# Optimization experiments

Hardware: AMD Instinct MI355X
Metric: run time of the kernel (lower is better)

The kernel has to match this reference:

```python
import jax, jax.numpy as jnp
import numpy as np

B, S, D, H = 4, 2048, 1024, 16
DK = D // H
NEG = -1000000000.0


def setup_inputs() -> dict:
    key = jax.random.key(0)
    ks = jax.random.split(key, 12)
    scale = 1.0 / np.sqrt(D)
    inp = {
        "query": jax.random.normal(ks[0], (B, S, D), jnp.float32),
        "key": jax.random.normal(ks[1], (B, S, D), jnp.float32),
        "value": jax.random.normal(ks[2], (B, S, D), jnp.float32),
        "mask": jax.random.randint(ks[3], (B, S, S), 0, 2, jnp.int32),
        "Wq": jax.random.normal(ks[4], (D, D), jnp.float32) * scale,
        "bq": jnp.zeros((D,), jnp.float32),
        "Wk": jax.random.normal(ks[5], (D, D), jnp.float32) * scale,
        "bk": jnp.zeros((D,), jnp.float32),
        "Wv": jax.random.normal(ks[6], (D, D), jnp.float32) * scale,
        "bv": jnp.zeros((D,), jnp.float32),
        "Wo": jax.random.normal(ks[7], (D, D), jnp.float32) * scale,
        "bo": jnp.zeros((D,), jnp.float32),
    }
    return inp


def _split_heads(x):
    # (B, S, D) -> (B, H, S, DK)
    return x.reshape(B, -1, H, DK).transpose(0, 2, 1, 3)


def reference(query, key, value, mask, Wq, bq, Wk, bk, Wv, bv, Wo, bo):
    q = _split_heads(query @ Wq.T + bq)
    k = _split_heads(key @ Wk.T + bk)
    v = _split_heads(value @ Wv.T + bv)
    scores = jnp.einsum('bhqd,bhkd->bhqk', q, k) / jnp.sqrt(jnp.float32(DK))
    scores = jnp.where(mask[:, None, :, :] == 0, NEG, scores)
    p_attn = jax.nn.softmax(scores, axis=-1)
    x = jnp.einsum('bhqk,bhkd->bhqd', p_attn, v)
    x = x.transpose(0, 2, 1, 3).reshape(B, -1, D)
    return x @ Wo.T + bo
```

## Files before the change

### kernel.cpp

```cpp
#include <hip/hip_runtime.h>

#define BDIM 4
#define SDIM 2048
#define DDIM 1024
#define HDIM 16
#define DKDIM 64
#define MDIM (BDIM*SDIM)

typedef __attribute__((ext_vector_type(8))) short bf16x8_t;
typedef __attribute__((ext_vector_type(4))) float f32x4_t;

__device__ __forceinline__ unsigned short f2bf(float f) {
    union { float f; unsigned u; } v; v.f = f;
    unsigned r = v.u + 0x7FFFu + ((v.u >> 16) & 1u);
    return (unsigned short)(r >> 16);
}

__device__ __forceinline__ unsigned pkbf(float a, float b) {
#if defined(__has_builtin) && __has_builtin(__builtin_amdgcn_cvt_pk_bf16_f32)
    auto v = __builtin_amdgcn_cvt_pk_bf16_f32(a, b);
    union { decltype(v) x; unsigned u; } cv; cv.x = v; return cv.u;
#else
    return (unsigned)f2bf(a) | ((unsigned)f2bf(b) << 16);
#endif
}

#if defined(__has_builtin) && __has_builtin(__builtin_amdgcn_exp2f)
#define EXP2F(x) __builtin_amdgcn_exp2f(x)
#else
#define EXP2F(x) __expf((x) * 0.69314718f)
#endif

#define QSCALE 0.18033688011112042f

__device__ __forceinline__ void gl_lds16(const void* g, void* l) {
    __builtin_amdgcn_global_load_lds(
        (const __attribute__((address_space(1))) unsigned int*)g,
        (__attribute__((address_space(3))) unsigned int*)l, 16, 0, 0);
}

__global__ void cvt3(const float* __restrict__ a, const float* __restrict__ b, const float* __restrict__ c,
                     unsigned short* __restrict__ oa, unsigned short* __restrict__ ob, unsigned short* __restrict__ oc,
                     int n4) {
    int i = blockIdx.x * blockDim.x + threadIdx.x;
    const float* s = blockIdx.y == 0 ? a : (blockIdx.y == 1 ? b : c);
    unsigned short* d = blockIdx.y == 0 ? oa : (blockIdx.y == 1 ? ob : oc);
    if (i < n4) {
        float4 v = ((const float4*)s)[i];
        ushort4 o;
        o.x = f2bf(v.x); o.y = f2bf(v.y); o.z = f2bf(v.z); o.w = f2bf(v.w);
        ((ushort4*)d)[i] = o;
    }
}

__global__ void cvt4(const float* __restrict__ a, const float* __restrict__ b,
                     const float* __restrict__ c, const float* __restrict__ e,
                     unsigned short* __restrict__ oa, unsigned short* __restrict__ ob,
                     unsigned short* __restrict__ oc, unsigned short* __restrict__ oe,
                     int n4) {
    int i = blockIdx.x * blockDim.x + threadIdx.x;
    const float* s = blockIdx.y == 0 ? a : (blockIdx.y == 1 ? b : (blockIdx.y == 2 ? c : e));
    unsigned short* d = blockIdx.y == 0 ? oa : (blockIdx.y == 1 ? ob : (blockIdx.y == 2 ? oc : oe));
    if (i < n4) {
        float4 v = ((const float4*)s)[i];
        ushort4 o;
        o.x = f2bf(v.x); o.y = f2bf(v.y); o.z = f2bf(v.z); o.w = f2bf(v.w);
        ((ushort4*)d)[i] = o;
    }
}

__global__ void pack_mask(const int* __restrict__ m, unsigned long long* __restrict__ bits) {
    int g = blockIdx.x * 256 + threadIdx.x;
    unsigned long long bal = __ballot(m[g] != 0);
    if ((threadIdx.x & 63) == 0) bits[g >> 6] = bal;
}

template<int OMODE>
__global__ __launch_bounds__(256) void gemm_nt(
    const unsigned short* __restrict__ A,
    const unsigned short* __restrict__ B,
    const float* __restrict__ bias,
    unsigned short* __restrict__ Cb,
    float* __restrict__ Cf,
    int M, int N, int K, float scale)
{
    __shared__ unsigned short As[128 * 32];
    __shared__ unsigned short Bs[128 * 32];
    const int tid = threadIdx.x;
    const int w = tid >> 6, lane = tid & 63;
    const int wr = w >> 1, wc = w & 1;
    const int quad = lane >> 4, l16 = lane & 15;
    const int bn = blockIdx.x, bm = blockIdx.y;

    const int rl = lane >> 2;
    const int cl = (((lane & 3) ^ ((rl >> 1) & 3)) * 8);
    const int sw = (l16 >> 1) & 3;
    const int c0 = w * 2;
    const unsigned short* gA = A + (size_t)(bm * 128 + c0 * 16 + rl) * K + cl;
    const unsigned short* gB = B + (size_t)(bn * 128 + c0 * 16 + rl) * K + cl;
    unsigned short* lA = As + c0 * 512 + lane * 8;
    unsigned short* lB = Bs + c0 * 512 + lane * 8;

    f32x4_t acc[4][4] = {};

    for (int k0 = 0; k0 < K; k0 += 32) {
        gl_lds16(gA, lA);
        gl_lds16(gA + (size_t)16 * K, lA + 16 * 32);
        gl_lds16(gB, lB);
        gl_lds16(gB + (size_t)16 * K, lB + 16 * 32);
        gA += 32; gB += 32;
        __syncthreads();
        bf16x8_t af[4], bfr[4];
#pragma unroll
        for (int mi = 0; mi < 4; ++mi)
            af[mi] = *(const bf16x8_t*)(As + (wr * 64 + mi * 16 + l16) * 32 + (quad ^ sw) * 8);
#pragma unroll
        for (int ni = 0; ni < 4; ++ni)
            bfr[ni] = *(const bf16x8_t*)(Bs + (wc * 64 + ni * 16 + l16) * 32 + (quad ^ sw) * 8);
#pragma unroll
        for (int mi = 0; mi < 4; ++mi)
#pragma unroll
            for (int ni = 0; ni < 4; ++ni)
                acc[mi][ni] = __builtin_amdgcn_mfma_f32_16x16x32_bf16(af[mi], bfr[ni], acc[mi][ni], 0, 0, 0);
        __syncthreads();
    }

#pragma unroll
    for (int mi = 0; mi < 4; ++mi) {
#pragma unroll
        for (int ni = 0; ni < 4; ++ni) {
            const int n = bn * 128 + wc * 64 + ni * 16 + l16;
            const int m0 = bm * 128 + wr * 64 + mi * 16 + quad * 4;
            const float bv = bias[n];
            if (OMODE == 1) {
                ushort4 pk;
                pk.x = f2bf((acc[mi][ni][0] + bv) * scale);
                pk.y = f2bf((acc[mi][ni][1] + bv) * scale);
                pk.z = f2bf((acc[mi][ni][2] + bv) * scale);
                pk.w = f2bf((acc[mi][ni][3] + bv) * scale);
                *(ushort4*)(Cb + (size_t)n * M + m0) = pk;
            } else {
#pragma unroll
                for (int r = 0; r < 4; ++r) {
                    const float v = (acc[mi][ni][r] + bv) * scale;
                    if (OMODE == 0) Cb[(size_t)(m0 + r) * N + n] = f2bf(v);
                    else            Cf[(size_t)(m0 + r) * N + n] = v;
                }
            }
        }
    }
}

__global__ __launch_bounds__(256) void attn_kernel(
    const unsigned short* __restrict__ Qp,
    const unsigned short* __restrict__ Kp,
    const unsigned short* __restrict__ Vt,
    const unsigned long long* __restrict__ mbits,
    unsigned short* __restrict__ Xa)
{
    __shared__ unsigned short SMEM[8192];
    unsigned short* const Ks = SMEM;
    unsigned short* const Vs = SMEM + 4096;

    const int tid = threadIdx.x, w = tid >> 6, lane = tid & 63;
    const int quad = lane >> 4, l16 = lane & 15;
    const int bx = blockIdx.x;
    const int h = bx & 15, qt = (bx >> 4) & 15, b = bx >> 8;
    const int q0 = qt * 128;
    const int rl = lane >> 2;
    const int cl = (((lane & 3) ^ ((rl >> 1) & 3)) * 8);
    const int sw = (l16 >> 1) & 3;
    const bool hi16 = (lane & 16) != 0;
    const bool hi32 = (lane & 32) != 0;
    const int idxA = (2 * (quad & 1) + (quad >> 1)) * 16 + l16;
    const int idxC = idxA ^ 16;

#pragma unroll
    for (int i = 0; i < 4; ++i) {
        const int cc = w * 4 + i;
        const int row = b * SDIM + q0 + (cc & 7) * 16 + rl;
        const int col = h * 64 + (cc >> 3) * 32 + cl;
        gl_lds16(Qp + (size_t)row * DDIM + col, SMEM + cc * 512 + lane * 8);
    }
    __syncthreads();
    bf16x8_t aq[2][2];
#pragma unroll
    for (int g = 0; g < 2; ++g)
#pragma unroll
        for (int kk = 0; kk < 2; ++kk)
            aq[g][kk] = *(const bf16x8_t*)(SMEM + (kk * 8 + w * 2 + g) * 512 + l16 * 32 + (quad ^ sw) * 8);

    const unsigned long long* mq0 = mbits + (size_t)(b * SDIM + q0 + w * 32 + l16) * 32;
    const unsigned long long* mq1 = mq0 + (size_t)16 * 32;

    f32x4_t o[2][4] = {};
    f32x4_t o4[2] = {};
    union { unsigned u[4]; bf16x8_t v; } ones;
    ones.u[0] = ones.u[1] = ones.u[2] = ones.u[3] = 0x3F803F80u;

    for (int kt = 0; kt < SDIM / 64; ++kt) {
        __syncthreads();
#pragma unroll
        for (int i = 0; i < 2; ++i) {
            const int cc = w * 2 + i;
            const int rowk = b * SDIM + kt * 64 + (cc & 3) * 16 + rl;
            const int colk = h * 64 + (cc >> 2) * 32 + cl;
            gl_lds16(Kp + (size_t)rowk * DDIM + colk, Ks + cc * 512 + lane * 8);
            const int rowv = h * 64 + (cc & 3) * 16 + rl;
            const int colv = b * SDIM + kt * 64 + (cc >> 2) * 32 + cl;
            gl_lds16(Vt + (size_t)rowv * MDIM + colv, Vs + cc * 512 + lane * 8);
        }
        __syncthreads();

        const unsigned long long sh0 = mq0[kt] >> (quad * 4);
        const unsigned long long sh1 = mq1[kt] >> (quad * 4);

        f32x4_t sf[2][4] = {};
#pragma unroll
        for (int kk = 0; kk < 2; ++kk) {
#pragma unroll
            for (int ni = 0; ni < 4; ++ni) {
                const bf16x8_t ak = *(const bf16x8_t*)(Ks + kk * 2048 + (ni * 16 + l16) * 32 + (quad ^ sw) * 8);
                sf[0][ni] = __builtin_amdgcn_mfma_f32_16x16x32_bf16(ak, aq[0][kk], sf[0][ni], 0, 0, 0);
                sf[1][ni] = __builtin_amdgcn_mfma_f32_16x16x32_bf16(ak, aq[1][kk], sf[1][ni], 0, 0, 0);
            }
        }

        unsigned P[2][4][2];
#pragma unroll
        for (int g = 0; g < 2; ++g) {
            const unsigned long long s = g ? sh1 : sh0;
            const unsigned mlo = (unsigned)s, mhi = (unsigned)(s >> 32);
#pragma unroll
            for (int ni = 0; ni < 4; ++ni) {
                const unsigned msel = (ni < 2) ? mlo : mhi;
                const int shf = (ni & 1) * 16;
                float p[4];
#pragma unroll
                for (int r = 0; r < 4; ++r) {
                    const bool on = (msel >> (shf + r)) & 1u;
                    p[r] = EXP2F(on ? sf[g][ni][r] : -1.0e9f);
                }
                P[g][ni][0] = pkbf(p[0], p[1]);
                P[g][ni][1] = pkbf(p[2], p[3]);
            }
        }

#pragma unroll
        for (int kk2 = 0; kk2 < 2; ++kk2) {
            bf16x8_t va[4];
#pragma unroll
            for (int ni = 0; ni < 4; ++ni)
                va[ni] = *(const bf16x8_t*)(Vs + kk2 * 2048 + (ni * 16 + l16) * 32 + (quad ^ sw) * 8);
#pragma unroll
            for (int g = 0; g < 2; ++g) {
                const unsigned Pa = P[g][kk2 * 2][0], Pb = P[g][kk2 * 2][1];
                const unsigned Pc = P[g][kk2 * 2 + 1][0], Pd = P[g][kk2 * 2 + 1][1];
                const int RA = hi16 ? (int)Pc : (int)Pa;
                const int RB = hi16 ? (int)Pd : (int)Pb;
                const int RC = hi16 ? (int)Pa : (int)Pc;
                const int RD = hi16 ? (int)Pb : (int)Pd;
                const int Av = __shfl(RA, idxA, 64);
                const int Bv = __shfl(RB, idxA, 64);
                const int Cv = __shfl(RC, idxC, 64);
                const int Dv = __shfl(RD, idxC, 64);
                union { unsigned u[4]; bf16x8_t v; } pf;
                pf.u[0] = (unsigned)(hi32 ? Cv : Av);
                pf.u[1] = (unsigned)(hi32 ? Dv : Bv);
                pf.u[2] = (unsigned)(hi32 ? Av : Cv);
                pf.u[3] = (unsigned)(hi32 ? Bv : Dv);
#pragma unroll
                for (int ni = 0; ni < 4; ++ni)
                    o[g][ni] = __builtin_amdgcn_mfma_f32_16x16x32_bf16(va[ni], pf.v, o[g][ni], 0, 0, 0);
                o4[g] = __builtin_amdgcn_mfma_f32_16x16x32_bf16(ones.v, pf.v, o4[g], 0, 0, 0);
            }
        }
    }

    __syncthreads();
    unsigned short* T = SMEM + w * 1152;
#pragma unroll
    for (int g = 0; g < 2; ++g) {
        const float rcp = 1.0f / o4[g][0];
#pragma unroll
        for (int ni = 0; ni < 4; ++ni) {
            uint2 pk;
            pk.x = pkbf(o[g][ni][0] * rcp, o[g][ni][1] * rcp);
            pk.y = pkbf(o[g][ni][2] * rcp, o[g][ni][3] * rcp);
            *(uint2*)&T[l16 * 72 + ni * 16 + quad * 4] = pk;
        }
        const int qrow = q0 + w * 32 + g * 16 + (lane >> 2);
        const int dkc = (lane & 3) * 16;
        const bf16x8_t r0 = *(const bf16x8_t*)&T[(lane >> 2) * 72 + dkc];
        const bf16x8_t r1 = *(const bf16x8_t*)&T[(lane >> 2) * 72 + dkc + 8];
        unsigned short* dst = Xa + (size_t)(b * SDIM + qrow) * DDIM + h * 64 + dkc;
        *(bf16x8_t*)dst = r0;
        *(bf16x8_t*)(dst + 8) = r1;
    }
}

extern "C" void kernel_launch(void* const* d_in, const int* in_sizes, int n_in,
                              void* d_out, int out_size, void* d_ws, size_t ws_size,
                              hipStream_t stream)
{
    const float* query = (const float*)d_in[0];
    const float* key   = (const float*)d_in[1];
    const float* value = (const float*)d_in[2];
    const int*   mask  = (const int*)d_in[3];
    const float* Wq = (const float*)d_in[4];  const float* bq = (const float*)d_in[5];
    const float* Wk = (const float*)d_in[6];  const float* bk = (const float*)d_in[7];
    const float* Wv = (const float*)d_in[8];  const float* bv = (const float*)d_in[9];
    const float* Wo = (const float*)d_in[10]; const float* bo = (const float*)d_in[11];

    const size_t MD = (size_t)MDIM * DDIM;
    const size_t DD = (size_t)DDIM * DDIM;

    unsigned short* qb  = (unsigned short*)d_ws;
    unsigned short* kb  = qb + MD;
    unsigned short* vb  = kb + MD;
    unsigned short* wqb = vb + MD;
    unsigned short* wkb = wqb + DD;
    unsigned short* wvb = wkb + DD;
    unsigned short* wob = wvb + DD;
    unsigned short* Qp  = wob + DD;
    unsigned short* Kp  = Qp + MD;
    unsigned short* Vt  = Kp + MD;
    unsigned short* Xa  = Vt + MD;
    unsigned long long* mbits = (unsigned long long*)qb;

    {
        const int n4m = (int)(MD / 4), n4d = (int)(DD / 4);
        dim3 g3((n4m + 255) / 256, 3), g4((n4d + 255) / 256, 4);
        cvt3<<<g3, 256, 0, stream>>>(query, key, value, qb, kb, vb, n4m);
        cvt4<<<g4, 256, 0, stream>>>(Wq, Wk, Wv, Wo, wqb, wkb, wvb, wob, n4d);
    }

    dim3 gg(DDIM / 128, MDIM / 128);
    gemm_nt<0><<<gg, 256, 0, stream>>>(qb, wqb, bq, Qp, nullptr, MDIM, DDIM, DDIM, QSCALE);
    gemm_nt<0><<<gg, 256, 0, stream>>>(kb, wkb, bk, Kp, nullptr, MDIM, DDIM, DDIM, 1.0f);
    gemm_nt<1><<<gg, 256, 0, stream>>>(vb, wvb, bv, Vt, nullptr, MDIM, DDIM, DDIM, 1.0f);

    pack_mask<<<(BDIM * SDIM * SDIM) / 256, 256, 0, stream>>>(mask, mbits);

    attn_kernel<<<BDIM * HDIM * (SDIM / 128), 256, 0, stream>>>(Qp, Kp, Vt, mbits, Xa);

    gemm_nt<2><<<gg, 256, 0, stream>>>(Xa, wob, bo, nullptr, (float*)d_out, MDIM, DDIM, DDIM, 1.0f);
}
```

Before: 490.2 us.

## Double-buffer LDS in GEMMs and attention, batch QKV projections in one launch

Adds double-buffered shared memory to the GEMM and attention loops so the global-to-LDS load of the next K tile (and next K/V tile plus mask words) is issued before computing on the current one, removing one barrier per iteration. The three Q/K/V projection GEMMs are merged into a single launch using blockIdx.z to select operands. The output GEMM becomes its own specialized kernel. The cost is doubled LDS per block, which may lower occupancy, plus extra barriers in the attention epilogue.

Result: faster. 463.8 us (-5.4%).

```diff
diff --git a/kernel.cpp b/kernel.cpp
--- a/kernel.cpp
+++ b/kernel.cpp
@@ -75,17 +75,25 @@
     if ((threadIdx.x & 63) == 0) bits[g >> 6] = bal;
 }
 
-template<int OMODE>
-__global__ __launch_bounds__(256) void gemm_nt(
-    const unsigned short* __restrict__ A,
-    const unsigned short* __restrict__ B,
-    const float* __restrict__ bias,
-    unsigned short* __restrict__ Cb,
-    float* __restrict__ Cf,
-    int M, int N, int K, float scale)
+__global__ __launch_bounds__(256) void gemm_qkv(
+    const unsigned short* __restrict__ A0, const unsigned short* __restrict__ A1,
+    const unsigned short* __restrict__ A2,
+    const unsigned short* __restrict__ B0, const unsigned short* __restrict__ B1,
+    const unsigned short* __restrict__ B2,
+    const float* __restrict__ bi0, const float* __restrict__ bi1, const float* __restrict__ bi2,
+    unsigned short* __restrict__ C0, unsigned short* __restrict__ C1,
+    unsigned short* __restrict__ C2)
 {
-    __shared__ unsigned short As[128 * 32];
-    __shared__ unsigned short Bs[128 * 32];
+    __shared__ unsigned short As[2][128 * 32];
+    __shared__ unsigned short Bs[2][128 * 32];
+    const int K = DDIM, M = MDIM, N = DDIM;
+    const int z = blockIdx.z;
+    const unsigned short* A = z == 0 ? A0 : (z == 1 ? A1 : A2);
+    const unsigned short* Bw = z == 0 ? B0 : (z == 1 ? B1 : B2);
+    const float* bias = z == 0 ? bi0 : (z == 1 ? bi1 : bi2);
+    unsigned short* Cb = z == 0 ? C0 : (z == 1 ? C1 : C2);
+    const float scale = z == 0 ? QSCALE : 1.0f;
+
     const int tid = threadIdx.x;
     const int w = tid >> 6, lane = tid & 63;
     const int wr = w >> 1, wc = w & 1;
@@ -97,32 +105,40 @@
     const int sw = (l16 >> 1) & 3;
     const int c0 = w * 2;
     const unsigned short* gA = A + (size_t)(bm * 128 + c0 * 16 + rl) * K + cl;
-    const unsigned short* gB = B + (size_t)(bn * 128 + c0 * 16 + rl) * K + cl;
-    unsigned short* lA = As + c0 * 512 + lane * 8;
-    unsigned short* lB = Bs + c0 * 512 + lane * 8;
+    const unsigned short* gB = Bw + (size_t)(bn * 128 + c0 * 16 + rl) * K + cl;
+    const int ldsoff = c0 * 512 + lane * 8;
 
     f32x4_t acc[4][4] = {};
 
+    gl_lds16(gA, &As[0][ldsoff]);
+    gl_lds16(gA + (size_t)16 * K, &As[0][ldsoff + 16 * 32]);
+    gl_lds16(gB, &Bs[0][ldsoff]);
+    gl_lds16(gB + (size_t)16 * K, &Bs[0][ldsoff + 16 * 32]);
+
+    int cur = 0;
     for (int k0 = 0; k0 < K; k0 += 32) {
-        gl_lds16(gA, lA);
-        gl_lds16(gA + (size_t)16 * K, lA + 16 * 32);
-        gl_lds16(gB, lB);
-        gl_lds16(gB + (size_t)16 * K, lB + 16 * 32);
-        gA += 32; gB += 32;
         __syncthreads();
+        if (k0 + 32 < K) {
+            const unsigned short* nA = gA + k0 + 32;
+            const unsigned short* nB = gB + k0 + 32;
+            gl_lds16(nA, &As[cur ^ 1][ldsoff]);
+            gl_lds16(nA + (size_t)16 * K, &As[cur ^ 1][ldsoff + 16 * 32]);
+            gl_lds16(nB, &Bs[cur ^ 1][ldsoff]);
+            gl_lds16(nB + (size_t)16 * K, &Bs[cur ^ 1][ldsoff + 16 * 32]);
+        }
         bf16x8_t af[4], bfr[4];
 #pragma unroll
         for (int mi = 0; mi < 4; ++mi)
-            af[mi] = *(const bf16x8_t*)(As + (wr * 64 + mi * 16 + l16) * 32 + (quad ^ sw) * 8);
+            af[mi] = *(const bf16x8_t*)(&As[cur][(wr * 64 + mi * 16 + l16) * 32 + (quad ^ sw) * 8]);
 #pragma unroll
         for (int ni = 0; ni < 4; ++ni)
-            bfr[ni] = *(const bf16x8_t*)(Bs + (wc * 64 + ni * 16 + l16) * 32 + (quad ^ sw) * 8);
+            bfr[ni] = *(const bf16x8_t*)(&Bs[cur][(wc * 64 + ni * 16 + l16) * 32 + (quad ^ sw) * 8]);
 #pragma unroll
         for (int mi = 0; mi < 4; ++mi)
 #pragma unroll
             for (int ni = 0; ni < 4; ++ni)
                 acc[mi][ni] = __builtin_amdgcn_mfma_f32_16x16x32_bf16(af[mi], bfr[ni], acc[mi][ni], 0, 0, 0);
-        __syncthreads();
+        cur ^= 1;
     }
 
 #pragma unroll
@@ -132,21 +148,88 @@
             const int n = bn * 128 + wc * 64 + ni * 16 + l16;
             const int m0 = bm * 128 + wr * 64 + mi * 16 + quad * 4;
             const float bv = bias[n];
-            if (OMODE == 1) {
+            if (z == 2) {
                 ushort4 pk;
-                pk.x = f2bf((acc[mi][ni][0] + bv) * scale);
-                pk.y = f2bf((acc[mi][ni][1] + bv) * scale);
-                pk.z = f2bf((acc[mi][ni][2] + bv) * scale);
-                pk.w = f2bf((acc[mi][ni][3] + bv) * scale);
+                pk.x = f2bf(acc[mi][ni][0] + bv);
+                pk.y = f2bf(acc[mi][ni][1] + bv);
+                pk.z = f2bf(acc[mi][ni][2] + bv);
+                pk.w = f2bf(acc[mi][ni][3] + bv);
                 *(ushort4*)(Cb + (size_t)n * M + m0) = pk;
             } else {
 #pragma unroll
-                for (int r = 0; r < 4; ++r) {
-                    const float v = (acc[mi][ni][r] + bv) * scale;
-                    if (OMODE == 0) Cb[(size_t)(m0 + r) * N + n] = f2bf(v);
-                    else            Cf[(size_t)(m0 + r) * N + n] = v;
-                }
+                for (int r = 0; r < 4; ++r)
+                    Cb[(size_t)(m0 + r) * N + n] = f2bf((acc[mi][ni][r] + bv) * scale);
             }
+        }
+    }
+}
+
+__global__ __launch_bounds__(256) void gemm_out(
+    const unsigned short* __restrict__ A,
+    const unsigned short* __restrict__ Bw,
+    const float* __restrict__ bias,
+    float* __restrict__ Cf)
+{
+    __shared__ unsigned short As[2][128 * 32];
+    __shared__ unsigned short Bs[2][128 * 32];
+    const int K = DDIM, N = DDIM;
+    const int tid = threadIdx.x;
+    const int w = tid >> 6, lane = tid & 63;
+    const int wr = w >> 1, wc = w & 1;
+    const int quad = lane >> 4, l16 = lane & 15;
+    const int bn = blockIdx.x, bm = blockIdx.y;
+
+    const int rl = lane >> 2;
+    const int cl = (((lane & 3) ^ ((rl >> 1) & 3)) * 8);
+    const int sw = (l16 >> 1) & 3;
+    const int c0 = w * 2;
+    const unsigned short* gA = A + (size_t)(bm * 128 + c0 * 16 + rl) * K + cl;
+    const unsigned short* gB = Bw + (size_t)(bn * 128 + c0 * 16 + rl) * K + cl;
+    const int ldsoff = c0 * 512 + lane * 8;
+
+    f32x4_t acc[4][4] = {};
+
+    gl_lds16(gA, &As[0][ldsoff]);
+    gl_lds16(gA + (size_t)16 * K, &As[0][ldsoff + 16 * 32]);
+    gl_lds16(gB, &Bs[0][ldsoff]);
+    gl_lds16(gB + (size_t)16 * K, &Bs[0][ldsoff + 16 * 32]);
+
+    int cur = 0;
+    for (int k0 = 0; k0 < K; k0 += 32) {
+        __syncthreads();
+        if (k0 + 32 < K) {
+            const unsigned short* nA = gA + k0 + 32;
+            const unsigned short* nB = gB + k0 + 32;
+            gl_lds16(nA, &As[cur ^ 1][ldsoff]);
+            gl_lds16(nA + (size_t)16 * K, &As[cur ^ 1][ldsoff + 16 * 32]);
+            gl_lds16(nB, &Bs[cur ^ 1][ldsoff]);
+            gl_lds16(nB + (size_t)16 * K, &Bs[cur ^ 1][ldsoff + 16 * 32]);
+        }
+        bf16x8_t af[4], bfr[4];
+#pragma unroll
+        for (int mi = 0; mi < 4; ++mi)
+            af[mi] = *(const bf16x8_t*)(&As[cur][(wr * 64 + mi * 16 + l16) * 32 + (quad ^ sw) * 8]);
+#pragma unroll
+        for (int ni = 0; ni < 4; ++ni)
+            bfr[ni] = *(const bf16x8_t*)(&Bs[cur][(wc * 64 + ni * 16 + l16) * 32 + (quad ^ sw) * 8]);
+#pragma unroll
+        for (int mi = 0; mi < 4; ++mi)
+#pragma unroll
+            for (int ni = 0; ni < 4; ++ni)
+                acc[mi][ni] = __builtin_amdgcn_mfma_f32_16x16x32_bf16(af[mi], bfr[ni], acc[mi][ni], 0, 0, 0);
+        cur ^= 1;
+    }
+
+#pragma unroll
+    for (int mi = 0; mi < 4; ++mi) {
+#pragma unroll
+        for (int ni = 0; ni < 4; ++ni) {
+            const int n = bn * 128 + wc * 64 + ni * 16 + l16;
+            const int m0 = bm * 128 + wr * 64 + mi * 16 + quad * 4;
+            const float bv = bias[n];
+#pragma unroll
+            for (int r = 0; r < 4; ++r)
+                Cf[(size_t)(m0 + r) * N + n] = acc[mi][ni][r] + bv;
         }
     }
 }
@@ -158,10 +241,7 @@
     const unsigned long long* __restrict__ mbits,
     unsigned short* __restrict__ Xa)
 {
-    __shared__ unsigned short SMEM[8192];
-    unsigned short* const Ks = SMEM;
-    unsigned short* const Vs = SMEM + 4096;
-
+    __shared__ unsigned short SMEM[16384];
     const int tid = threadIdx.x, w = tid >> 6, lane = tid & 63;
     const int quad = lane >> 4, l16 = lane & 15;
     const int bx = blockIdx.x;
@@ -189,38 +269,60 @@
 #pragma unroll
         for (int kk = 0; kk < 2; ++kk)
             aq[g][kk] = *(const bf16x8_t*)(SMEM + (kk * 8 + w * 2 + g) * 512 + l16 * 32 + (quad ^ sw) * 8);
+    __syncthreads();
 
     const unsigned long long* mq0 = mbits + (size_t)(b * SDIM + q0 + w * 32 + l16) * 32;
     const unsigned long long* mq1 = mq0 + (size_t)16 * 32;
+
+#pragma unroll
+    for (int i = 0; i < 2; ++i) {
+        const int cc = w * 2 + i;
+        const int rowk = b * SDIM + (cc & 3) * 16 + rl;
+        const int colk = h * 64 + (cc >> 2) * 32 + cl;
+        gl_lds16(Kp + (size_t)rowk * DDIM + colk, SMEM + cc * 512 + lane * 8);
+        const int rowv = h * 64 + (cc & 3) * 16 + rl;
+        const int colv = b * SDIM + (cc >> 2) * 32 + cl;
+        gl_lds16(Vt + (size_t)rowv * MDIM + colv, SMEM + 8192 + cc * 512 + lane * 8);
+    }
+    unsigned long long nm0 = mq0[0], nm1 = mq1[0];
 
     f32x4_t o[2][4] = {};
     f32x4_t o4[2] = {};
     union { unsigned u[4]; bf16x8_t v; } ones;
     ones.u[0] = ones.u[1] = ones.u[2] = ones.u[3] = 0x3F803F80u;
 
+    int cur = 0;
     for (int kt = 0; kt < SDIM / 64; ++kt) {
         __syncthreads();
-#pragma unroll
-        for (int i = 0; i < 2; ++i) {
-            const int cc = w * 2 + i;
-            const int rowk = b * SDIM + kt * 64 + (cc & 3) * 16 + rl;
-            const int colk = h * 64 + (cc >> 2) * 32 + cl;
-            gl_lds16(Kp + (size_t)rowk * DDIM + colk, Ks + cc * 512 + lane * 8);
-            const int rowv = h * 64 + (cc & 3) * 16 + rl;
-            const int colv = b * SDIM + kt * 64 + (cc >> 2) * 32 + cl;
-            gl_lds16(Vt + (size_t)rowv * MDIM + colv, Vs + cc * 512 + lane * 8);
-        }
-        __syncthreads();
-
-        const unsigned long long sh0 = mq0[kt] >> (quad * 4);
-        const unsigned long long sh1 = mq1[kt] >> (quad * 4);
+
+        const unsigned long long sh0 = nm0 >> (quad * 4);
+        const unsigned long long sh1 = nm1 >> (quad * 4);
+
+        if (kt + 1 < SDIM / 64) {
+            const int nb = cur ^ 1;
+#pragma unroll
+            for (int i = 0; i < 2; ++i) {
+                const int cc = w * 2 + i;
+                const int rowk = b * SDIM + (kt + 1) * 64 + (cc & 3) * 16 + rl;
+                const int colk = h * 64 + (cc >> 2) * 32 + cl;
+                gl_lds16(Kp + (size_t)rowk * DDIM + colk, SMEM + nb * 4096 + cc * 512 + lane * 8);
+                const int rowv = h * 64 + (cc & 3) * 16 + rl;
+                const int colv = b * SDIM + (kt + 1) * 64 + (cc >> 2) * 32 + cl;
+                gl_lds16(Vt + (size_t)rowv * MDIM + colv, SMEM + 8192 + nb * 4096 + cc * 512 + lane * 8);
+            }
+            nm0 = mq0[kt + 1];
+            nm1 = mq1[kt + 1];
+        }
+
+        const unsigned short* Ksb = SMEM + cur * 4096;
+        const unsigned short* Vsb = SMEM + 8192 + cur * 4096;
 
         f32x4_t sf[2][4] = {};
 #pragma unroll
         for (int kk = 0; kk < 2; ++kk) {
 #pragma unroll
             for (int ni = 0; ni < 4; ++ni) {
-                const bf16x8_t ak = *(const bf16x8_t*)(Ks + kk * 2048 + (ni * 16 + l16) * 32 + (quad ^ sw) * 8);
+                const bf16x8_t ak = *(const bf16x8_t*)(Ksb + kk * 2048 + (ni * 16 + l16) * 32 + (quad ^ sw) * 8);
                 sf[0][ni] = __builtin_amdgcn_mfma_f32_16x16x32_bf16(ak, aq[0][kk], sf[0][ni], 0, 0, 0);
                 sf[1][ni] = __builtin_amdgcn_mfma_f32_16x16x32_bf16(ak, aq[1][kk], sf[1][ni], 0, 0, 0);
             }
@@ -251,7 +353,7 @@
             bf16x8_t va[4];
 #pragma unroll
             for (int ni = 0; ni < 4; ++ni)
-                va[ni] = *(const bf16x8_t*)(Vs + kk2 * 2048 + (ni * 16 + l16) * 32 + (quad ^ sw) * 8);
+                va[ni] = *(const bf16x8_t*)(Vsb + kk2 * 2048 + (ni * 16 + l16) * 32 + (quad ^ sw) * 8);
 #pragma unroll
             for (int g = 0; g < 2; ++g) {
                 const unsigned Pa = P[g][kk2 * 2][0], Pb = P[g][kk2 * 2][1];
@@ -275,6 +377,7 @@
                 o4[g] = __builtin_amdgcn_mfma_f32_16x16x32_bf16(ones.v, pf.v, o4[g], 0, 0, 0);
             }
         }
+        cur ^= 1;
     }
 
     __syncthreads();
@@ -291,11 +394,13 @@
         }
         const int qrow = q0 + w * 32 + g * 16 + (lane >> 2);
         const int dkc = (lane & 3) * 16;
+        __syncthreads();
         const bf16x8_t r0 = *(const bf16x8_t*)&T[(lane >> 2) * 72 + dkc];
         const bf16x8_t r1 = *(const bf16x8_t*)&T[(lane >> 2) * 72 + dkc + 8];
         unsigned short* dst = Xa + (size_t)(b * SDIM + qrow) * DDIM + h * 64 + dkc;
         *(bf16x8_t*)dst = r0;
         *(bf16x8_t*)(dst + 8) = r1;
+        __syncthreads();
     }
 }
 
@@ -335,14 +440,13 @@
         cvt4<<<g4, 256, 0, stream>>>(Wq, Wk, Wv, Wo, wqb, wkb, wvb, wob, n4d);
     }
 
+    dim3 gq(DDIM / 128, MDIM / 128, 3);
+    gemm_qkv<<<gq, 256, 0, stream>>>(qb, kb, vb, wqb, wkb, wvb, bq, bk, bv, Qp, Kp, Vt);
+
+    pack_mask<<<(BDIM * SDIM * SDIM) / 256, 256, 0, stream>>>(mask, mbits);
+
+    attn_kernel<<<BDIM * HDIM * (SDIM / 128), 256, 0, stream>>>(Qp, Kp, Vt, mbits, Xa);
+
     dim3 gg(DDIM / 128, MDIM / 128);
-    gemm_nt<0><<<gg, 256, 0, stream>>>(qb, wqb, bq, Qp, nullptr, MDIM, DDIM, DDIM, QSCALE);
-    gemm_nt<0><<<gg, 256, 0, stream>>>(kb, wkb, bk, Kp, nullptr, MDIM, DDIM, DDIM, 1.0f);
-    gemm_nt<1><<<gg, 256, 0, stream>>>(vb, wvb, bv, Vt, nullptr, MDIM, DDIM, DDIM, 1.0f);
-
-    pack_mask<<<(BDIM * SDIM * SDIM) / 256, 256, 0, stream>>>(mask, mbits);
-
-    attn_kernel<<<BDIM * HDIM * (SDIM / 128), 256, 0, stream>>>(Qp, Kp, Vt, mbits, Xa);
-
-    gemm_nt<2><<<gg, 256, 0, stream>>>(Xa, wob, bo, nullptr, (float*)d_out, MDIM, DDIM, DDIM, 1.0f);
-}
+    gemm_out<<<gg, 256, 0, stream>>>(Xa, wob, bo, (float*)d_out);
+}
```
